# Kernel optimization log

Hardware: AMD Instinct MI355X
Metric: run time of the kernel (lower is better)

The kernel has to match this reference:

```python
import jax, jax.numpy as jnp
import numpy as np

# Workspace layout (static slice bounds, per init_kwargs)
SS, SE = 0, 512        # spoke
HPS, HPE = 512, 768    # hub private
HSS, HSE = 768, 1024   # hub shared
TS, TE = 1024, 1088    # tag
HS, HE = 512, 1024     # full hub (priv + shared) for the read path

B, T, D_STATE, D_MODEL, D_LATENT = 8, 4096, 1088, 1024, 128


def setup_inputs() -> dict:
    key = jax.random.key(0)
    ks = jax.random.split(key, 10)
    scale = 0.02  # typical init scale for learned projections
    return {
        "S": jax.random.normal(ks[0], (B, T, D_STATE), jnp.float32),
        "w_spoke": jax.random.normal(ks[1], (B, T, SE - SS), jnp.float32),
        "w_hub_priv": jax.random.normal(ks[2], (B, T, HPE - HPS), jnp.float32),
        "w_hub_shared": jax.random.normal(ks[3], (B, T, HSE - HSS), jnp.float32),
        "tag": jax.random.normal(ks[4], (B, T, TE - TS), jnp.float32),
        "W_read": jax.random.normal(ks[5], (D_MODEL, D_STATE), jnp.float32) * scale,
        "cache": jnp.zeros((B, T, D_LATENT), jnp.float32),
        "latent": jax.random.normal(ks[6], (B, T, D_LATENT), jnp.float32),
        "Wk": jax.random.normal(ks[7], (D_MODEL, D_LATENT), jnp.float32) * scale,
        "Wv": jax.random.normal(ks[8], (D_MODEL, D_LATENT), jnp.float32) * scale,
    }


def reference(S, w_spoke, w_hub_priv, w_hub_shared, tag, W_read, cache, latent, Wk, Wv):
    # --- fused_workspace_write: four independent slice-adds into S ---
    S = S.at[:, :, SS:SE].add(w_spoke)
    S = S.at[:, :, HPS:HPE].add(w_hub_priv)
    S = S.at[:, :, HSS:HSE].add(w_hub_shared)
    S = S.at[:, :, TS:TE].add(tag)

    # --- fused_workspace_read: concat(spoke, hub, tag) then F.linear(., W_read) ---
    readable = jnp.concatenate(
        [S[:, :, SS:SE], S[:, :, HS:HE], S[:, :, TS:TE]], axis=-1
    )  # (B, T, D_STATE)
    out = jnp.einsum("btr,dr->btd", readable, W_read)  # (B, T, D_MODEL)

    # --- CWTLatentCache.update: overwrite latents at start_position=0 ---
    cache = jax.lax.dynamic_update_slice(cache, latent, (0, 0, 0))

    # --- K/V reconstruction from compressed latents via up-projections ---
    k = jnp.einsum("btl,dl->btd", cache, Wk)  # (B, T, D_MODEL)
    v = jnp.einsum("btl,dl->btd", cache, Wv)  # (B, T, D_MODEL)
    return (out, k, v)
```

## Files before the change

### kernel.cpp

```cpp
#include <hip/hip_runtime.h>

typedef __attribute__((ext_vector_type(8))) _Float16 half8;
typedef __attribute__((ext_vector_type(2))) __fp16 half2r;
typedef __attribute__((ext_vector_type(4))) float f32x4;

#define AS1 __attribute__((address_space(1)))
#define AS3 __attribute__((address_space(3)))

union H2U { half2r h; unsigned int u; };
union Frag { half8 v; unsigned long long d[2]; };

__device__ __forceinline__ unsigned int pk(float a, float b) {
    H2U x; x.h = __builtin_amdgcn_cvt_pkrtz(a, b); return x.u;
}

__device__ __forceinline__ void gload_lds16(const void* g, void* l) {
    __builtin_amdgcn_global_load_lds((const AS1 unsigned int*)g,
                                     (AS3 unsigned int*)l, 16, 0, 0);
}

#define W1_ROWB 2176
#define WS2_OFF 2228224
#define W2_ROWB 256
#define A_ROWB  2176
#define TBUF    65536

__device__ __forceinline__ void pick_w(int ks, const float* wsp, const float* whp,
                                       const float* whs, const float* wtg,
                                       const float*& wbase, int& wstr, int& wko) {
    if (ks < 8)       { wbase = wsp; wstr = 512; wko = ks * 64; }
    else if (ks < 12) { wbase = whp; wstr = 256; wko = ks * 64 - 512; }
    else if (ks < 16) { wbase = whs; wstr = 256; wko = ks * 64 - 768; }
    else              { wbase = wtg; wstr = 64;  wko = 0; }
}

__global__ __launch_bounds__(256) void prep_w(const float* __restrict__ Wr,
                                              const float* __restrict__ Wk,
                                              const float* __restrict__ Wv,
                                              char* __restrict__ ws) {
    int id = blockIdx.x * 256 + threadIdx.x;
    if (id < 272 * 1024) {
        int n = id / 272;
        int k = (id % 272) * 4;
        f32x4 w = *(const f32x4*)(Wr + (size_t)n * 1088 + k);
        uint2 q; q.x = pk(w.x, w.y); q.y = pk(w.z, w.w);
        size_t off = (size_t)n * W1_ROWB + ((k >> 6) << 7)
                   + (((k & 63) << 1) ^ ((n & 7) << 4));
        *(uint2*)(ws + off) = q;
    } else {
        int j = id - 272 * 1024;
        int r = j >> 5;
        int k = (j & 31) << 2;
        const float* src = (r < 1024) ? (Wk + (size_t)r * 128 + k)
                                      : (Wv + (size_t)(r - 1024) * 128 + k);
        f32x4 w = *(const f32x4*)src;
        uint2 q; q.x = pk(w.x, w.y); q.y = pk(w.z, w.w);
        size_t off = WS2_OFF + (size_t)r * W2_ROWB + ((k >> 6) << 7)
                   + (((k & 63) << 1) ^ ((r & 7) << 4));
        *(uint2*)(ws + off) = q;
    }
}

__global__ __launch_bounds__(256)
void fuse_a(const float* __restrict__ S, const float* __restrict__ wsp,
            const float* __restrict__ whp, const float* __restrict__ whs,
            const float* __restrict__ wtg, char* __restrict__ a16) {
    int u = blockIdx.x * 256 + threadIdx.x;
    int row = u / 272;
    int rem = u % 272;
    int ks = rem >> 4;
    int k4 = (rem & 15) << 2;

    const float* wbase; int wstr, wko;
    pick_w(ks, wsp, whp, whs, wtg, wbase, wstr, wko);

    f32x4 s4 = *(const f32x4*)(S + (size_t)row * 1088 + ks * 64 + k4);
    f32x4 w4 = *(const f32x4*)(wbase + (size_t)row * wstr + wko + k4);
    uint2 q; q.x = pk(s4.x + w4.x, s4.y + w4.y);
             q.y = pk(s4.z + w4.z, s4.w + w4.w);
    size_t off = (size_t)row * A_ROWB + (ks << 7)
               + (((k4) << 1) ^ ((row & 7) << 4));
    *(uint2*)(a16 + off) = q;
}

__global__ __launch_bounds__(512, 2)
void gemm_read(const char* __restrict__ wsA, const char* __restrict__ wws,
               float* __restrict__ out) {
    extern __shared__ char lds[];

    int bid = blockIdx.x;
    int wg   = (bid & 7) * 64 + (bid >> 3);
    int mblk = wg >> 2, nblk = wg & 3;
    int m0 = mblk << 8, n0 = nblk << 8;

    int tid = threadIdx.x;
    int lane = tid & 63, wid = tid >> 6;
    int wm = (wid >> 2) << 7, wn = (wid & 3) << 6;
    int lp = lane & 15, lg = lane >> 4;

    f32x4 acc[8][4] = {};

#define STAGE(T, DL) do {                                                  \
        const char* garow = wsA + (size_t)m0 * A_ROWB + (size_t)(T) * 128; \
        const char* gbrow = wws + (size_t)n0 * W1_ROWB + (size_t)(T) * 128;\
        _Pragma("unroll")                                                  \
        for (int c = 0; c < 4; ++c) {                                      \
            int s = c * 8192 + tid * 16;                                   \
            gload_lds16(garow + (size_t)(s >> 7) * A_ROWB + (s & 127),     \
                        (DL) + s);                                         \
        }                                                                  \
        _Pragma("unroll")                                                  \
        for (int c = 0; c < 4; ++c) {                                      \
            int s = c * 8192 + tid * 16;                                   \
            gload_lds16(gbrow + (size_t)(s >> 7) * W1_ROWB + (s & 127),    \
                        (DL) + 32768 + s);                                 \
        }                                                                  \
    } while (0)

#define COMPUTE(AL, BL) do {                                               \
        _Pragma("unroll")                                                  \
        for (int b = 0; b < 2; ++b) {                                      \
            Frag af[8], bf[4];                                             \
            _Pragma("unroll")                                              \
            for (int f = 0; f < 8; ++f) {                                  \
                int ra = wm + f * 16 + lp;  int xa = (ra & 7) << 4;        \
                af[f].d[0] = *(const unsigned long long*)((AL) + (ra << 7) + ((b * 64 + lg * 8) ^ xa));      \
                af[f].d[1] = *(const unsigned long long*)((AL) + (ra << 7) + ((b * 64 + 32 + lg * 8) ^ xa)); \
            }                                                              \
            _Pragma("unroll")                                              \
            for (int f = 0; f < 4; ++f) {                                  \
                int rb = wn + f * 16 + lp;  int xb = (rb & 7) << 4;        \
                bf[f].d[0] = *(const unsigned long long*)((BL) + (rb << 7) + ((b * 64 + lg * 8) ^ xb));      \
                bf[f].d[1] = *(const unsigned long long*)((BL) + (rb << 7) + ((b * 64 + 32 + lg * 8) ^ xb)); \
            }                                                              \
            __builtin_amdgcn_s_setprio(1);                                 \
            _Pragma("unroll")                                              \
            for (int i = 0; i < 8; ++i)                                    \
                _Pragma("unroll")                                          \
                for (int j = 0; j < 4; ++j)                                \
                    acc[i][j] = __builtin_amdgcn_mfma_f32_16x16x32_f16(af[i].v, bf[j].v, acc[i][j], 0, 0, 0); \
            __builtin_amdgcn_s_setprio(0);                                 \
        }                                                                  \
    } while (0)

    STAGE(0, lds);

    for (int t = 0; t < 17; ++t) {
        if (t < 16) {
            STAGE(t + 1, lds + ((t + 1) & 1) * TBUF);
            asm volatile("s_waitcnt vmcnt(8)" ::: "memory");
        } else {
            asm volatile("s_waitcnt vmcnt(0)" ::: "memory");
        }
        __builtin_amdgcn_s_barrier();
        const char* cb = lds + (t & 1) * TBUF;
        COMPUTE(cb, cb + 32768);
        __builtin_amdgcn_s_barrier();
    }

    #pragma unroll
    for (int i = 0; i < 8; ++i)
        #pragma unroll
        for (int j = 0; j < 4; ++j) {
            int row = m0 + wm + i * 16 + (lg << 2);
            int col = n0 + wn + j * 16 + lp;
            float* p = out + (size_t)row * 1024 + col;
            #pragma unroll
            for (int r = 0; r < 4; ++r) p[(size_t)r * 1024] = acc[i][j][r];
        }
#undef STAGE
#undef COMPUTE
}

__global__ __launch_bounds__(256, 2)
void gemm_kv(const float* __restrict__ lat, const char* __restrict__ ws2,
             float* __restrict__ outk, float* __restrict__ outv) {
    __shared__ char lds[32768];
    char* Al = lds;
    char* Bl = lds + 16384;

    int bid = blockIdx.x;
    int wg   = (bid & 7) * 512 + (bid >> 3);
    int mblk = wg >> 4, nb = wg & 15;
    int m0 = mblk << 7;
    int nrow0 = nb << 7;
    float* out = (nb < 8) ? outk : outv;
    int n0 = (nb & 7) << 7;

    int tid = threadIdx.x;
    int lane = tid & 63, wid = tid >> 6;
    int wm = (wid >> 1) << 6, wn = (wid & 1) << 6;
    int lp = lane & 15, lg = lane >> 4;

    f32x4 acc[4][4] = {};

    for (int ks = 0; ks < 2; ++ks) {
        __syncthreads();
        {
            const char* wrow = ws2 + (size_t)nrow0 * W2_ROWB + ks * 128;
            #pragma unroll
            for (int c = 0; c < 4; ++c) {
                int s = c * 4096 + wid * 1024 + lane * 16;
                int n = s >> 7, cb = s & 127;
                gload_lds16(wrow + (size_t)n * W2_ROWB + cb,
                            Bl + c * 4096 + wid * 1024);
            }
        }
        #pragma unroll
        for (int i = 0; i < 8; ++i) {
            int u = i * 256 + tid;
            int row = u >> 4;
            int k4 = (u & 15) << 2;
            f32x4 s4 = *(const f32x4*)(lat + (size_t)(m0 + row) * 128 + ks * 64 + k4);
            uint2 q; q.x = pk(s4.x, s4.y); q.y = pk(s4.z, s4.w);
            *(uint2*)(Al + (row << 7) + ((k4 << 1) ^ ((row & 7) << 4))) = q;
        }
        __syncthreads();

        #pragma unroll
        for (int b = 0; b < 2; ++b) {
            Frag af[4], bf[4];
            #pragma unroll
            for (int f = 0; f < 4; ++f) {
                int ra = wm + f * 16 + lp;  int xa = (ra & 7) << 4;
                af[f].d[0] = *(const unsigned long long*)(Al + (ra << 7) + ((b * 64 + lg * 8) ^ xa));
                af[f].d[1] = *(const unsigned long long*)(Al + (ra << 7) + ((b * 64 + 32 + lg * 8) ^ xa));
                int rb = wn + f * 16 + lp;  int xb = (rb & 7) << 4;
                bf[f].d[0] = *(const unsigned long long*)(Bl + (rb << 7) + ((b * 64 + lg * 8) ^ xb));
                bf[f].d[1] = *(const unsigned long long*)(Bl + (rb << 7) + ((b * 64 + 32 + lg * 8) ^ xb));
            }
            #pragma unroll
            for (int i = 0; i < 4; ++i)
                #pragma unroll
                for (int j = 0; j < 4; ++j)
                    acc[i][j] = __builtin_amdgcn_mfma_f32_16x16x32_f16(af[i].v, bf[j].v, acc[i][j], 0, 0, 0);
        }
    }

    #pragma unroll
    for (int i = 0; i < 4; ++i)
        #pragma unroll
        for (int j = 0; j < 4; ++j) {
            int row = m0 + wm + i * 16 + (lg << 2);
            int col = n0 + wn + j * 16 + lp;
            float* p = out + (size_t)row * 1024 + col;
            #pragma unroll
            for (int r = 0; r < 4; ++r) p[(size_t)r * 1024] = acc[i][j][r];
        }
}

extern "C" void kernel_launch(void* const* d_in, const int* in_sizes, int n_in,
                              void* d_out, int out_size, void* d_ws, size_t ws_size,
                              hipStream_t stream) {
    const float* S   = (const float*)d_in[0];
    const float* wsp = (const float*)d_in[1];
    const float* whp = (const float*)d_in[2];
    const float* whs = (const float*)d_in[3];
    const float* wtg = (const float*)d_in[4];
    const float* Wr  = (const float*)d_in[5];
    const float* lat = (const float*)d_in[7];
    const float* Wk  = (const float*)d_in[8];
    const float* Wv  = (const float*)d_in[9];
    float* out = (float*)d_out;
    char*  ws  = (char*)d_ws;

    static bool lds_init = false;
    if (!lds_init) {
        hipFuncSetAttribute(reinterpret_cast<const void*>(gemm_read),
                            hipFuncAttributeMaxDynamicSharedMemorySize, 2 * TBUF);
        lds_init = true;
    }

    char* a16 = (char*)(out + 67108864ull);

    hipLaunchKernelGGL(prep_w, dim3(1344), dim3(256), 0, stream, Wr, Wk, Wv, ws);
    hipLaunchKernelGGL(fuse_a, dim3(34816), dim3(256), 0, stream,
                       S, wsp, whp, whs, wtg, a16);
    hipLaunchKernelGGL(gemm_read, dim3(512), dim3(512), 2 * TBUF, stream,
                       a16, ws, out);
    hipLaunchKernelGGL(gemm_kv, dim3(4096), dim3(256), 0, stream,
                       lat, ws + WS2_OFF, out + 33554432ull, out + 67108864ull);
}
```

Baseline: 275.2 us.

## Pre-tile A and W into contiguous 16KB blocks and interleave staging with MFMA phases

The fused A operand and the W_read weights are now written in a tiled layout: 128-row by 64-k blocks of 16KB each, with a new XOR swizzle chosen so each lane can read a full 16-byte fragment in one LDS access. Each stage then becomes two fully contiguous 8KB loads per quarter instead of strided row loads. The main loop is split into four sub-phases so the next tile's global-to-LDS loads are issued between MFMA groups, which is meant to overlap memory with compute and reduce register pressure from holding fragments. The cost is many more barriers per k-step and a layout that every producer kernel must match.

Result: faster. 255.0 us (-7.4%).

```diff
diff --git a/kernel.cpp b/kernel.cpp
--- a/kernel.cpp
+++ b/kernel.cpp
@@ -19,11 +19,8 @@
                                      (AS3 unsigned int*)l, 16, 0, 0);
 }
 
-#define W1_ROWB 2176
 #define WS2_OFF 2228224
 #define W2_ROWB 256
-#define A_ROWB  2176
-#define TBUF    65536
 
 __device__ __forceinline__ void pick_w(int ks, const float* wsp, const float* whp,
                                        const float* whs, const float* wtg,
@@ -32,6 +29,12 @@
     else if (ks < 12) { wbase = whp; wstr = 256; wko = ks * 64 - 512; }
     else if (ks < 16) { wbase = whs; wstr = 256; wko = ks * 64 - 768; }
     else              { wbase = wtg; wstr = 64;  wko = 0; }
+}
+
+__device__ __forceinline__ size_t pf_addr(int r, int kt) {
+    int kh = kt >> 5, k32 = kt & 31;
+    int u = (k32 & 15) >> 2, pos8 = (k32 >> 4) << 3;
+    return ((size_t)r << 7) + ((size_t)((((kh << 2) | u) ^ ((r >> 1) & 7)) << 4)) + pos8;
 }
 
 __global__ __launch_bounds__(256) void prep_w(const float* __restrict__ Wr,
@@ -44,8 +47,8 @@
         int k = (id % 272) * 4;
         f32x4 w = *(const f32x4*)(Wr + (size_t)n * 1088 + k);
         uint2 q; q.x = pk(w.x, w.y); q.y = pk(w.z, w.w);
-        size_t off = (size_t)n * W1_ROWB + ((k >> 6) << 7)
-                   + (((k & 63) << 1) ^ ((n & 7) << 4));
+        int t = k >> 6;
+        size_t off = ((size_t)((n >> 7) * 17 + t) << 14) + pf_addr(n & 127, k & 63);
         *(uint2*)(ws + off) = q;
     } else {
         int j = id - 272 * 1024;
@@ -78,13 +81,12 @@
     f32x4 w4 = *(const f32x4*)(wbase + (size_t)row * wstr + wko + k4);
     uint2 q; q.x = pk(s4.x + w4.x, s4.y + w4.y);
              q.y = pk(s4.z + w4.z, s4.w + w4.w);
-    size_t off = (size_t)row * A_ROWB + (ks << 7)
-               + (((k4) << 1) ^ ((row & 7) << 4));
+    size_t off = ((size_t)((row >> 7) * 17 + ks) << 14) + pf_addr(row & 127, k4);
     *(uint2*)(a16 + off) = q;
 }
 
 __global__ __launch_bounds__(512, 2)
-void gemm_read(const char* __restrict__ wsA, const char* __restrict__ wws,
+void gemm_read(const char* __restrict__ a16, const char* __restrict__ wws,
                float* __restrict__ out) {
     extern __shared__ char lds[];
 
@@ -98,64 +100,93 @@
     int wm = (wid >> 2) << 7, wn = (wid & 3) << 6;
     int lp = lane & 15, lg = lane >> 4;
 
+    int aoff = (wid >> 2) * 16384;
+    int boff = 32768 + (wn >> 7) * 16384;
+    int cb64 = wn & 64;
+
+    const char* srcH[4];
+    srcH[0] = a16 + ((size_t)((m0 >> 7) * 17) << 14);
+    srcH[1] = srcH[0] + (17 << 14);
+    srcH[2] = wws + ((size_t)((n0 >> 7) * 17) << 14);
+    srcH[3] = srcH[2] + (17 << 14);
+
     f32x4 acc[8][4] = {};
-
-#define STAGE(T, DL) do {                                                  \
-        const char* garow = wsA + (size_t)m0 * A_ROWB + (size_t)(T) * 128; \
-        const char* gbrow = wws + (size_t)n0 * W1_ROWB + (size_t)(T) * 128;\
+    Frag af[4], bf[4];
+
+#define STAGE(T, H, DB) do {                                               \
+        const char* s_ = srcH[H] + ((size_t)(T) << 14);                    \
+        char* d_ = lds + (DB) + (H) * 16384;                               \
+        gload_lds16(s_ + tid * 16, d_ + tid * 16);                         \
+        gload_lds16(s_ + 8192 + tid * 16, d_ + 8192 + tid * 16);           \
+    } while (0)
+
+#define LOADA(MH, KH, BB) do {                                             \
         _Pragma("unroll")                                                  \
-        for (int c = 0; c < 4; ++c) {                                      \
-            int s = c * 8192 + tid * 16;                                   \
-            gload_lds16(garow + (size_t)(s >> 7) * A_ROWB + (s & 127),     \
-                        (DL) + s);                                         \
-        }                                                                  \
-        _Pragma("unroll")                                                  \
-        for (int c = 0; c < 4; ++c) {                                      \
-            int s = c * 8192 + tid * 16;                                   \
-            gload_lds16(gbrow + (size_t)(s >> 7) * W1_ROWB + (s & 127),    \
-                        (DL) + 32768 + s);                                 \
+        for (int f = 0; f < 4; ++f) {                                      \
+            int r_ = (MH) * 64 + f * 16 + lp;                              \
+            af[f] = *(const Frag*)(lds + (BB) + aoff + (r_ << 7)           \
+                     + ((((((KH) << 2) | lg) ^ ((r_ >> 1) & 7))) << 4));   \
         }                                                                  \
     } while (0)
 
-#define COMPUTE(AL, BL) do {                                               \
+#define LOADB(KH, BB) do {                                                 \
         _Pragma("unroll")                                                  \
-        for (int b = 0; b < 2; ++b) {                                      \
-            Frag af[8], bf[4];                                             \
-            _Pragma("unroll")                                              \
-            for (int f = 0; f < 8; ++f) {                                  \
-                int ra = wm + f * 16 + lp;  int xa = (ra & 7) << 4;        \
-                af[f].d[0] = *(const unsigned long long*)((AL) + (ra << 7) + ((b * 64 + lg * 8) ^ xa));      \
-                af[f].d[1] = *(const unsigned long long*)((AL) + (ra << 7) + ((b * 64 + 32 + lg * 8) ^ xa)); \
-            }                                                              \
-            _Pragma("unroll")                                              \
-            for (int f = 0; f < 4; ++f) {                                  \
-                int rb = wn + f * 16 + lp;  int xb = (rb & 7) << 4;        \
-                bf[f].d[0] = *(const unsigned long long*)((BL) + (rb << 7) + ((b * 64 + lg * 8) ^ xb));      \
-                bf[f].d[1] = *(const unsigned long long*)((BL) + (rb << 7) + ((b * 64 + 32 + lg * 8) ^ xb)); \
-            }                                                              \
-            __builtin_amdgcn_s_setprio(1);                                 \
-            _Pragma("unroll")                                              \
-            for (int i = 0; i < 8; ++i)                                    \
-                _Pragma("unroll")                                          \
-                for (int j = 0; j < 4; ++j)                                \
-                    acc[i][j] = __builtin_amdgcn_mfma_f32_16x16x32_f16(af[i].v, bf[j].v, acc[i][j], 0, 0, 0); \
-            __builtin_amdgcn_s_setprio(0);                                 \
+        for (int g = 0; g < 4; ++g) {                                      \
+            int c_ = cb64 + g * 16 + lp;                                   \
+            bf[g] = *(const Frag*)(lds + (BB) + boff + (c_ << 7)           \
+                     + ((((((KH) << 2) | lg) ^ ((c_ >> 1) & 7))) << 4));   \
         }                                                                  \
     } while (0)
 
-    STAGE(0, lds);
-
-    for (int t = 0; t < 17; ++t) {
-        if (t < 16) {
-            STAGE(t + 1, lds + ((t + 1) & 1) * TBUF);
-            asm volatile("s_waitcnt vmcnt(8)" ::: "memory");
-        } else {
-            asm volatile("s_waitcnt vmcnt(0)" ::: "memory");
-        }
-        __builtin_amdgcn_s_barrier();
-        const char* cb = lds + (t & 1) * TBUF;
-        COMPUTE(cb, cb + 32768);
-        __builtin_amdgcn_s_barrier();
+#define MFMA16(MH) do {                                                    \
+        __builtin_amdgcn_s_setprio(1);                                     \
+        _Pragma("unroll")                                                  \
+        for (int f = 0; f < 4; ++f)                                        \
+            _Pragma("unroll")                                              \
+            for (int g = 0; g < 4; ++g)                                    \
+                acc[(MH) * 4 + f][g] = __builtin_amdgcn_mfma_f32_16x16x32_f16( \
+                    af[f].v, bf[g].v, acc[(MH) * 4 + f][g], 0, 0, 0);      \
+        __builtin_amdgcn_s_setprio(0);                                     \
+    } while (0)
+
+    STAGE(0, 0, 0); STAGE(0, 1, 0); STAGE(0, 2, 0); STAGE(0, 3, 0);
+
+    for (int t = 0; t < 16; ++t) {
+        int BB = (t & 1) << 16;
+        int NB = BB ^ 65536;
+        STAGE(t + 1, 0, NB);
+        asm volatile("s_waitcnt vmcnt(2)" ::: "memory");
+        __builtin_amdgcn_s_barrier();
+        LOADB(0, BB); LOADA(0, 0, BB);
+        MFMA16(0);
+        __builtin_amdgcn_s_barrier();
+        LOADA(1, 0, BB);
+        STAGE(t + 1, 1, NB);
+        __builtin_amdgcn_s_barrier();
+        MFMA16(1);
+        __builtin_amdgcn_s_barrier();
+        LOADB(1, BB); LOADA(0, 1, BB);
+        STAGE(t + 1, 2, NB);
+        __builtin_amdgcn_s_barrier();
+        MFMA16(0);
+        __builtin_amdgcn_s_barrier();
+        LOADA(1, 1, BB);
+        STAGE(t + 1, 3, NB);
+        __builtin_amdgcn_s_barrier();
+        MFMA16(1);
+        __builtin_amdgcn_s_barrier();
+    }
+    {
+        const int BB = 0;
+        asm volatile("s_waitcnt vmcnt(0)" ::: "memory");
+        __builtin_amdgcn_s_barrier();
+        LOADB(0, BB); LOADA(0, 0, BB); MFMA16(0);
+        __builtin_amdgcn_s_barrier();
+        LOADA(1, 0, BB); MFMA16(1);
+        __builtin_amdgcn_s_barrier();
+        LOADB(1, BB); LOADA(0, 1, BB); MFMA16(0);
+        __builtin_amdgcn_s_barrier();
+        LOADA(1, 1, BB); MFMA16(1);
     }
 
     #pragma unroll
@@ -169,7 +200,9 @@
             for (int r = 0; r < 4; ++r) p[(size_t)r * 1024] = acc[i][j][r];
         }
 #undef STAGE
-#undef COMPUTE
+#undef LOADA
+#undef LOADB
+#undef MFMA16
 }
 
 __global__ __launch_bounds__(256, 2)
@@ -267,7 +300,7 @@
     static bool lds_init = false;
     if (!lds_init) {
         hipFuncSetAttribute(reinterpret_cast<const void*>(gemm_read),
-                            hipFuncAttributeMaxDynamicSharedMemorySize, 2 * TBUF);
+                            hipFuncAttributeMaxDynamicSharedMemorySize, 131072);
         lds_init = true;
     }
 
@@ -276,7 +309,7 @@
     hipLaunchKernelGGL(prep_w, dim3(1344), dim3(256), 0, stream, Wr, Wk, Wv, ws);
     hipLaunchKernelGGL(fuse_a, dim3(34816), dim3(256), 0, stream,
                        S, wsp, whp, whs, wtg, a16);
-    hipLaunchKernelGGL(gemm_read, dim3(512), dim3(512), 2 * TBUF, stream,
+    hipLaunchKernelGGL(gemm_read, dim3(512), dim3(512), 131072, stream,
                        a16, ws, out);
     hipLaunchKernelGGL(gemm_kv, dim3(4096), dim3(256), 0, stream,
                        lat, ws + WS2_OFF, out + 33554432ull, out + 67108864ull);
```
